# Kernel tuning notes

Measured on AMD Instinct MI355X. Metric: run time of the kernel, lower is better.

Reference implementation:

```python
import jax, jax.numpy as jnp
import numpy as np

N_ATOMS = 200000
N_EDGES = 6400000
N_TYPES = 4
COULOMB = 14.399645478425668  # e^2 / (4 pi eps0) in eV*Angstrom
P_EXP = 0.23
A0 = 0.4685


def _phi(r, c, da):
    # r: (E,), c: (4,), da: (4, E) -> (E,)
    return jnp.sum(c[:, None] * jnp.exp(-r * da), axis=0)


def _dphi(r, c, da):
    return jnp.sum(-c[:, None] * da * jnp.exp(-r * da), axis=0)


def _d2phi(r, c, da):
    return jnp.sum(c[:, None] * da ** 2 * jnp.exp(-r * da), axis=0)


def setup_inputs() -> dict:
    key = jax.random.key(0)
    k1, k2, k3, k4 = jax.random.split(key, 4)
    rij = jax.random.uniform(k1, (N_EDGES,), dtype=jnp.float32) * 2.0 + 0.1
    first_atom = jax.random.randint(k2, (N_EDGES,), 0, N_ATOMS, dtype=jnp.int32)
    second_atom = jax.random.randint(k3, (N_EDGES,), 0, N_ATOMS, dtype=jnp.int32)
    atom_type_index = jax.random.randint(k4, (N_ATOMS,), 0, N_TYPES, dtype=jnp.int32)
    # ASE covalent radii for H, C, N, O (Angstrom) and atomic numbers
    covalent_radii = jnp.array([0.31, 0.76, 0.71, 0.66], dtype=jnp.float32)
    atomic_numbers = jnp.array([1.0, 6.0, 7.0, 8.0], dtype=jnp.float32)
    return {
        "rij": rij,
        "covalent_radii": covalent_radii,
        "atomic_numbers": atomic_numbers,
        "first_atom": first_atom,
        "second_atom": second_atom,
        "atom_type_index": atom_type_index,
        "n_atoms": N_ATOMS,
    }


def reference(rij, covalent_radii, atomic_numbers, first_atom, second_atom, atom_type_index, n_atoms):
    # ZBL 4-term exponential screening coefficients
    c = jnp.array([0.02817, 0.28022, 0.50986, 0.18175], dtype=rij.dtype)
    d = jnp.array([0.20162, 0.4029, 0.94229, 3.1998], dtype=rij.dtype)

    ti = atom_type_index[first_atom]   # (E,)
    tj = atom_type_index[second_atom]  # (E,)
    zi = atomic_numbers[ti]
    zj = atomic_numbers[tj]
    rc = covalent_radii[ti] + covalent_radii[tj]  # outer cutoff per pair

    a = A0 / (zi ** P_EXP + zj ** P_EXP)  # (E,)
    da = d[:, None] / a                    # (4, E)
    factor = COULOMB * zi * zj             # (E,)

    # energy at rij
    e = factor / rij * _phi(rij, c, da)

    # switching polynomial matched at rc (r1 = 0)
    phi_c = _phi(rc, c, da)
    dphi_c = _dphi(rc, c, da)
    d2phi_c = _d2phi(rc, c, da)
    ec = factor / rc * phi_c
    dec = factor / rc * (-phi_c / rc + dphi_c)
    d2ec = factor / rc * (d2phi_c - 2.0 / rc * dphi_c + 2.0 * phi_c / rc ** 2)

    A = (-3.0 * dec + rc * d2ec) / rc ** 2
    B = (2.0 * dec - rc * d2ec) / rc ** 3
    C = -ec + rc * dec / 2.0 - rc * rc * d2ec / 12.0

    e = e + A / 3.0 * rij ** 3 + B / 4.0 * rij ** 4 + C
    e = e / 2.0
    e = jnp.where(rij > rc, jnp.zeros_like(e), e)

    # scatter pair energies onto first atom of each pair
    e_nodes = jax.ops.segment_sum(e, first_atom, num_segments=n_atoms)
    return e_nodes
```

## Files before the change

### kernel.cpp

```cpp
#include <hip/hip_runtime.h>

#define TPB_PACK  256
#define P1_BLOCKS 512
#define P1_TPB    512
#define BUCKET_BITS 10
#define BS (1 << BUCKET_BITS)
#define P2_TPB    256
#define P2_S      8
#define CMAX      64
#define NB_MAX    256

__global__ __launch_bounds__(TPB_PACK) void zbl_pack(
    const int* __restrict__ types, unsigned int* __restrict__ packed,
    int natoms, int nwords)
{
    int w = blockIdx.x * TPB_PACK + threadIdx.x;
    if (w >= nwords) return;
    int base = w << 4;
    unsigned int word = 0;
    #pragma unroll
    for (int j = 0; j < 16; ++j) {
        int i = base + j;
        unsigned int t = (i < natoms) ? (unsigned int)types[i] : 0u;
        word |= (t & 3u) << (2 * j);
    }
    packed[w] = word;
}

__global__ __launch_bounds__(P1_TPB) void zbl_bin(
    const float* __restrict__ rij,
    const float* __restrict__ rcov,
    const float* __restrict__ znum,
    const int*  __restrict__ fa,
    const int*  __restrict__ sa,
    const unsigned int* __restrict__ packed,
    int2*  __restrict__ regions,
    int*   __restrict__ counts,
    float* __restrict__ fallback,
    int E, int nquad, int natoms, int nwords, int NB, int C, int chunkQ)
{
    extern __shared__ unsigned int s_packed[];
    __shared__ float tab[9][16];
    __shared__ int scnt[NB_MAX];

    for (int w = threadIdx.x; w < nwords; w += P1_TPB)
        s_packed[w] = packed[w];
    for (int t = threadIdx.x; t < NB; t += P1_TPB) scnt[t] = 0;

    if (threadIdx.x < 16) {
        const float cc[4] = {0.02817f, 0.28022f, 0.50986f, 0.18175f};
        const float dd[4] = {0.20162f, 0.4029f, 0.94229f, 3.1998f};
        const float COUL = 14.399645478425668f;
        int t = threadIdx.x;
        int ti = t >> 2, tj = t & 3;
        float zi = znum[ti], zj = znum[tj];
        float rc = rcov[ti] + rcov[tj];
        float a = 0.4685f / (powf(zi, 0.23f) + powf(zj, 0.23f));
        float inva = 1.0f / a;
        float factor = COUL * zi * zj;
        float da[4], ee[4];
        float phi = 0.0f, dphi = 0.0f, d2phi = 0.0f;
        #pragma unroll
        for (int k = 0; k < 4; ++k) {
            da[k] = dd[k] * inva;
            ee[k] = expf(-rc * da[k]);
            phi   += cc[k] * ee[k];
            dphi  -= cc[k] * da[k] * ee[k];
            d2phi += cc[k] * da[k] * da[k] * ee[k];
        }
        float invrc = 1.0f / rc;
        float ec   = factor * invrc * phi;
        float dec  = factor * invrc * (-phi * invrc + dphi);
        float d2ec = factor * invrc * (d2phi - 2.0f * invrc * dphi + 2.0f * phi * invrc * invrc);
        float A = (-3.0f * dec + rc * d2ec) * invrc * invrc;
        float B = (2.0f * dec - rc * d2ec) * invrc * invrc * invrc;
        float Cc = -ec + 0.5f * rc * dec - rc * rc * d2ec * (1.0f / 12.0f);
        const float L2E = 1.4426950408889634f;
        tab[0][t] = 0.5f * factor;
        tab[1][t] = rc;
        tab[2][t] = -da[0] * L2E;
        tab[3][t] = -da[1] * L2E;
        tab[4][t] = -da[2] * L2E;
        tab[5][t] = -da[3] * L2E;
        tab[6][t] = A * (1.0f / 6.0f);
        tab[7][t] = B * 0.125f;
        tab[8][t] = Cc * 0.5f;
    }
    __syncthreads();

    const float lc0 = -5.1497481f;
    const float lc1 = -1.8353434f;
    const float lc2 = -0.9718340f;
    const float lc3 = -2.4600449f;

    const float4* rij4 = (const float4*)rij;
    const int4*   fa4  = (const int4*)fa;
    const int4*   sa4  = (const int4*)sa;

    int q0 = blockIdx.x * chunkQ;
    int q1 = q0 + chunkQ; if (q1 > nquad) q1 = nquad;

    for (int q = q0 + threadIdx.x; q < q1; q += P1_TPB) {
        float4 rv = rij4[q];
        int4   iv = fa4[q];
        int4   jv = sa4[q];
        float ra[4] = {rv.x, rv.y, rv.z, rv.w};
        int   ia[4] = {iv.x, iv.y, iv.z, iv.w};
        int   ja[4] = {jv.x, jv.y, jv.z, jv.w};
        int   ta[4];
        #pragma unroll
        for (int k = 0; k < 4; ++k) {
            int i = ia[k], j = ja[k];
            unsigned int wi = s_packed[i >> 4], wj = s_packed[j >> 4];
            unsigned int ti = (wi >> ((i & 15) * 2)) & 3u;
            unsigned int tj = (wj >> ((j & 15) * 2)) & 3u;
            ta[k] = (int)((ti << 2) | tj);
        }
        #pragma unroll
        for (int k = 0; k < 4; ++k) {
            int t = ta[k];
            float r = ra[k];
            if (r <= tab[1][t]) {
                float p = __builtin_amdgcn_exp2f(__builtin_fmaf(r, tab[2][t], lc0))
                        + __builtin_amdgcn_exp2f(__builtin_fmaf(r, tab[3][t], lc1))
                        + __builtin_amdgcn_exp2f(__builtin_fmaf(r, tab[4][t], lc2))
                        + __builtin_amdgcn_exp2f(__builtin_fmaf(r, tab[5][t], lc3));
                float r3 = r * r * r;
                float poly = __builtin_fmaf(__builtin_fmaf(tab[7][t], r, tab[6][t]), r3, tab[8][t]);
                float e = __builtin_fmaf(tab[0][t] * p, __builtin_amdgcn_rcpf(r), poly);
                int atom = ia[k];
                int b = atom >> BUCKET_BITS;
                int slot = atomicAdd(&scnt[b], 1);
                if (slot < C)
                    regions[((size_t)blockIdx.x * NB + b) * (size_t)C + slot] =
                        make_int2(__float_as_int(e), atom);
                else
                    unsafeAtomicAdd(&fallback[atom], e);
            }
        }
    }

    if (blockIdx.x == 0) {
        for (int idx = nquad * 4 + threadIdx.x; idx < E; idx += P1_TPB) {
            int i = fa[idx], j = sa[idx];
            unsigned int wi = s_packed[i >> 4], wj = s_packed[j >> 4];
            int t = (int)((((wi >> ((i & 15) * 2)) & 3u) << 2) |
                           ((wj >> ((j & 15) * 2)) & 3u));
            float r = rij[idx];
            if (r <= tab[1][t]) {
                float p = __builtin_amdgcn_exp2f(__builtin_fmaf(r, tab[2][t], lc0))
                        + __builtin_amdgcn_exp2f(__builtin_fmaf(r, tab[3][t], lc1))
                        + __builtin_amdgcn_exp2f(__builtin_fmaf(r, tab[4][t], lc2))
                        + __builtin_amdgcn_exp2f(__builtin_fmaf(r, tab[5][t], lc3));
                float r3 = r * r * r;
                float poly = __builtin_fmaf(__builtin_fmaf(tab[7][t], r, tab[6][t]), r3, tab[8][t]);
                float e = __builtin_fmaf(tab[0][t] * p, __builtin_amdgcn_rcpf(r), poly);
                int b = i >> BUCKET_BITS;
                int slot = atomicAdd(&scnt[b], 1);
                if (slot < C)
                    regions[((size_t)blockIdx.x * NB + b) * (size_t)C + slot] =
                        make_int2(__float_as_int(e), i);
                else
                    unsafeAtomicAdd(&fallback[i], e);
            }
        }
    }

    __syncthreads();
    if (C > 0)
        for (int t = threadIdx.x; t < NB; t += P1_TPB)
            counts[t * P1_BLOCKS + blockIdx.x] = min(scnt[t], C);
}

__global__ __launch_bounds__(P2_TPB) void zbl_agg(
    const int2* __restrict__ regions,
    const int*  __restrict__ counts,
    const float* __restrict__ fallback,
    float* __restrict__ out,
    int natoms, int NB, int C)
{
    const int PPS = P1_BLOCKS / P2_S;
    __shared__ float acc[BS];
    __shared__ int s_n[PPS];

    int b = blockIdx.x;
    int s = blockIdx.y;
    if (threadIdx.x < PPS)
        s_n[threadIdx.x] = counts[b * P1_BLOCKS + s + P2_S * threadIdx.x];
    for (int i = threadIdx.x; i < BS; i += P2_TPB) acc[i] = 0.0f;
    __syncthreads();

    int wave = threadIdx.x >> 6;
    int lane = threadIdx.x & 63;
    for (int pi = wave; pi < PPS; pi += (P2_TPB >> 6)) {
        int n = s_n[pi];
        int p = s + P2_S * pi;
        if (lane < n) {
            int2 r = regions[((size_t)p * NB + b) * (size_t)C + lane];
            atomicAdd(&acc[r.y & (BS - 1)], __int_as_float(r.x));
        }
    }
    __syncthreads();

    int abase = b << BUCKET_BITS;
    for (int i = threadIdx.x; i < BS; i += P2_TPB) {
        int atom = abase + i;
        if (atom < natoms) {
            float v = acc[i];
            if (s == 0) v += fallback[atom];
            unsafeAtomicAdd(&out[atom], v);
        }
    }
}

extern "C" void kernel_launch(void* const* d_in, const int* in_sizes, int n_in,
                              void* d_out, int out_size, void* d_ws, size_t ws_size,
                              hipStream_t stream) {
    const float* rij  = (const float*)d_in[0];
    const float* rcov = (const float*)d_in[1];
    const float* znum = (const float*)d_in[2];
    const int*   fa   = (const int*)d_in[3];
    const int*   sa   = (const int*)d_in[4];
    const int*   types= (const int*)d_in[5];
    float* out = (float*)d_out;
    int E = in_sizes[0];
    int natoms = out_size;
    int nquad = E / 4;
    int nwords = (natoms + 15) / 16;
    int NB = (natoms + BS - 1) >> BUCKET_BITS;
    if (NB > NB_MAX) NB = NB_MAX;
    int chunkQ = (nquad + P1_BLOCKS - 1) / P1_BLOCKS;

    size_t packed_bytes = ((size_t)nwords * 4 + 255) & ~(size_t)255;
    size_t cnt_bytes    = ((size_t)NB * P1_BLOCKS * 4 + 255) & ~(size_t)255;
    size_t fb_bytes     = ((size_t)natoms * 4 + 255) & ~(size_t)255;
    unsigned int* packed = (unsigned int*)d_ws;
    int*   counts   = (int*)((char*)d_ws + packed_bytes);
    float* fallback = (float*)((char*)d_ws + packed_bytes + cnt_bytes);
    int2*  regions  = (int2*)((char*)d_ws + packed_bytes + cnt_bytes + fb_bytes);

    long long avail = (long long)ws_size - (long long)(packed_bytes + cnt_bytes + fb_bytes);
    int C = 0;
    if (avail > 0) C = (int)(avail / ((long long)P1_BLOCKS * (long long)NB * 8));
    if (C > CMAX) C = CMAX;

    size_t smem = (size_t)nwords * sizeof(unsigned int);

    zbl_pack<<<(nwords + TPB_PACK - 1) / TPB_PACK, TPB_PACK, 0, stream>>>(
        types, packed, natoms, nwords);

    if (C >= 1) {
        hipMemsetAsync(fallback, 0, fb_bytes, stream);
        hipMemsetAsync(d_out, 0, (size_t)natoms * 4, stream);
        zbl_bin<<<P1_BLOCKS, P1_TPB, smem, stream>>>(
            rij, rcov, znum, fa, sa, packed, regions, counts, fallback,
            E, nquad, natoms, nwords, NB, C, chunkQ);
        dim3 g2(NB, P2_S);
        zbl_agg<<<g2, P2_TPB, 0, stream>>>(
            regions, counts, fallback, out, natoms, NB, C);
    } else {
        hipMemsetAsync(d_out, 0, (size_t)natoms * 4, stream);
        zbl_bin<<<P1_BLOCKS, P1_TPB, smem, stream>>>(
            rij, rcov, znum, fa, sa, packed, regions, counts, out,
            E, nquad, natoms, nwords, NB, 0, chunkQ);
    }
}
```

Before: 188.8 us.

## Pack bin records into 32-bit words, split producers, add deterministic reduction pass

Each binned record now packs the energy with its low 10 mantissa bits rounded off and replaced by the atom's in-bucket index, halving region traffic. The binning kernel runs more blocks, and each block keeps two per-wave-group counter sets, so there are more producer regions and less LDS atomic contention. Aggregation writes per-slice partials instead of doing global atomic adds, and a new reduction kernel sums the partials plus the fallback, which removes the output memset. In exchange, energy precision is lost in the low mantissa bits and an extra kernel launch is added.

```diff
diff --git a/kernel.cpp b/kernel.cpp
--- a/kernel.cpp
+++ b/kernel.cpp
@@ -1,13 +1,17 @@
 #include <hip/hip_runtime.h>
 
 #define TPB_PACK  256
-#define P1_BLOCKS 512
+#define P1_BLOCKS 768
 #define P1_TPB    512
+#define REP       2
+#define PRODUCERS (P1_BLOCKS * REP)
 #define BUCKET_BITS 10
 #define BS (1 << BUCKET_BITS)
 #define P2_TPB    256
 #define P2_S      8
-#define CMAX      64
+#define PPS       (PRODUCERS / P2_S)
+#define TPB_RED   256
+#define CMAX      48
 #define NB_MAX    256
 
 __global__ __launch_bounds__(TPB_PACK) void zbl_pack(
@@ -34,18 +38,18 @@
     const int*  __restrict__ fa,
     const int*  __restrict__ sa,
     const unsigned int* __restrict__ packed,
-    int2*  __restrict__ regions,
+    unsigned int* __restrict__ regions,
     int*   __restrict__ counts,
     float* __restrict__ fallback,
     int E, int nquad, int natoms, int nwords, int NB, int C, int chunkQ)
 {
     extern __shared__ unsigned int s_packed[];
     __shared__ float tab[9][16];
-    __shared__ int scnt[NB_MAX];
+    __shared__ int scnt[REP * NB_MAX];
 
     for (int w = threadIdx.x; w < nwords; w += P1_TPB)
         s_packed[w] = packed[w];
-    for (int t = threadIdx.x; t < NB; t += P1_TPB) scnt[t] = 0;
+    for (int t = threadIdx.x; t < REP * NB; t += P1_TPB) scnt[t] = 0;
 
     if (threadIdx.x < 16) {
         const float cc[4] = {0.02817f, 0.28022f, 0.50986f, 0.18175f};
@@ -97,6 +101,9 @@
     const int4*   fa4  = (const int4*)fa;
     const int4*   sa4  = (const int4*)sa;
 
+    int rep = (threadIdx.x >> 6) & (REP - 1);
+    int vp  = blockIdx.x * REP + rep;
+
     int q0 = blockIdx.x * chunkQ;
     int q1 = q0 + chunkQ; if (q1 > nquad) q1 = nquad;
 
@@ -130,12 +137,14 @@
                 float e = __builtin_fmaf(tab[0][t] * p, __builtin_amdgcn_rcpf(r), poly);
                 int atom = ia[k];
                 int b = atom >> BUCKET_BITS;
-                int slot = atomicAdd(&scnt[b], 1);
-                if (slot < C)
-                    regions[((size_t)blockIdx.x * NB + b) * (size_t)C + slot] =
-                        make_int2(__float_as_int(e), atom);
-                else
+                int slot = atomicAdd(&scnt[rep * NB + b], 1);
+                if (slot < C) {
+                    unsigned rec = ((__float_as_uint(e) + 0x200u) & 0xFFFFFC00u)
+                                 | (unsigned)(atom & (BS - 1));
+                    regions[((size_t)vp * NB + b) * (size_t)C + slot] = rec;
+                } else {
                     unsafeAtomicAdd(&fallback[atom], e);
+                }
             }
         }
     }
@@ -156,61 +165,76 @@
                 float poly = __builtin_fmaf(__builtin_fmaf(tab[7][t], r, tab[6][t]), r3, tab[8][t]);
                 float e = __builtin_fmaf(tab[0][t] * p, __builtin_amdgcn_rcpf(r), poly);
                 int b = i >> BUCKET_BITS;
-                int slot = atomicAdd(&scnt[b], 1);
-                if (slot < C)
-                    regions[((size_t)blockIdx.x * NB + b) * (size_t)C + slot] =
-                        make_int2(__float_as_int(e), i);
-                else
+                int slot = atomicAdd(&scnt[rep * NB + b], 1);
+                if (slot < C) {
+                    unsigned rec = ((__float_as_uint(e) + 0x200u) & 0xFFFFFC00u)
+                                 | (unsigned)(i & (BS - 1));
+                    regions[((size_t)vp * NB + b) * (size_t)C + slot] = rec;
+                } else {
                     unsafeAtomicAdd(&fallback[i], e);
+                }
             }
         }
     }
 
     __syncthreads();
-    if (C > 0)
-        for (int t = threadIdx.x; t < NB; t += P1_TPB)
-            counts[t * P1_BLOCKS + blockIdx.x] = min(scnt[t], C);
+    if (C > 0) {
+        for (int t = threadIdx.x; t < REP * NB; t += P1_TPB) {
+            int rr = t / NB, b = t - rr * NB;
+            counts[(size_t)b * PRODUCERS + blockIdx.x * REP + rr] = min(scnt[t], C);
+        }
+    }
 }
 
 __global__ __launch_bounds__(P2_TPB) void zbl_agg(
-    const int2* __restrict__ regions,
+    const unsigned int* __restrict__ regions,
     const int*  __restrict__ counts,
-    const float* __restrict__ fallback,
-    float* __restrict__ out,
-    int natoms, int NB, int C)
-{
-    const int PPS = P1_BLOCKS / P2_S;
+    float* __restrict__ partials,
+    int NB, int C)
+{
     __shared__ float acc[BS];
     __shared__ int s_n[PPS];
 
     int b = blockIdx.x;
     int s = blockIdx.y;
-    if (threadIdx.x < PPS)
-        s_n[threadIdx.x] = counts[b * P1_BLOCKS + s + P2_S * threadIdx.x];
     for (int i = threadIdx.x; i < BS; i += P2_TPB) acc[i] = 0.0f;
+    for (int pi = threadIdx.x; pi < PPS; pi += P2_TPB)
+        s_n[pi] = counts[(size_t)b * PRODUCERS + pi * P2_S + s];
     __syncthreads();
 
     int wave = threadIdx.x >> 6;
     int lane = threadIdx.x & 63;
     for (int pi = wave; pi < PPS; pi += (P2_TPB >> 6)) {
         int n = s_n[pi];
-        int p = s + P2_S * pi;
-        if (lane < n) {
-            int2 r = regions[((size_t)p * NB + b) * (size_t)C + lane];
-            atomicAdd(&acc[r.y & (BS - 1)], __int_as_float(r.x));
-        }
-    }
-    __syncthreads();
-
-    int abase = b << BUCKET_BITS;
-    for (int i = threadIdx.x; i < BS; i += P2_TPB) {
-        int atom = abase + i;
-        if (atom < natoms) {
-            float v = acc[i];
-            if (s == 0) v += fallback[atom];
-            unsafeAtomicAdd(&out[atom], v);
-        }
-    }
+        int vp = pi * P2_S + s;
+        size_t base = ((size_t)vp * NB + b) * (size_t)C;
+        for (int t = lane; t < n; t += 64) {
+            unsigned rec = regions[base + t];
+            atomicAdd(&acc[rec & (BS - 1)],
+                      __uint_as_float(rec & ~(unsigned)(BS - 1)));
+        }
+    }
+    __syncthreads();
+
+    float* dst = partials + ((size_t)b * P2_S + s) * BS;
+    for (int i = threadIdx.x; i < BS; i += P2_TPB)
+        dst[i] = acc[i];
+}
+
+__global__ __launch_bounds__(TPB_RED) void zbl_red(
+    const float* __restrict__ partials,
+    const float* __restrict__ fallback,
+    float* __restrict__ out,
+    int natoms)
+{
+    int atom = blockIdx.x * TPB_RED + threadIdx.x;
+    if (atom >= natoms) return;
+    int b = atom >> BUCKET_BITS, i = atom & (BS - 1);
+    float s = fallback[atom];
+    const float* p = partials + (size_t)b * P2_S * BS + i;
+    #pragma unroll
+    for (int k = 0; k < P2_S; ++k) s += p[(size_t)k * BS];
+    out[atom] = s;
 }
 
 extern "C" void kernel_launch(void* const* d_in, const int* in_sizes, int n_in,
@@ -228,20 +252,23 @@
     int nquad = E / 4;
     int nwords = (natoms + 15) / 16;
     int NB = (natoms + BS - 1) >> BUCKET_BITS;
-    if (NB > NB_MAX) NB = NB_MAX;
     int chunkQ = (nquad + P1_BLOCKS - 1) / P1_BLOCKS;
 
     size_t packed_bytes = ((size_t)nwords * 4 + 255) & ~(size_t)255;
-    size_t cnt_bytes    = ((size_t)NB * P1_BLOCKS * 4 + 255) & ~(size_t)255;
+    size_t cnt_bytes    = ((size_t)NB * PRODUCERS * 4 + 255) & ~(size_t)255;
     size_t fb_bytes     = ((size_t)natoms * 4 + 255) & ~(size_t)255;
+    size_t part_bytes   = ((size_t)NB * P2_S * BS * 4 + 255) & ~(size_t)255;
     unsigned int* packed = (unsigned int*)d_ws;
-    int*   counts   = (int*)((char*)d_ws + packed_bytes);
+    int*   counts   = (int*)  ((char*)d_ws + packed_bytes);
     float* fallback = (float*)((char*)d_ws + packed_bytes + cnt_bytes);
-    int2*  regions  = (int2*)((char*)d_ws + packed_bytes + cnt_bytes + fb_bytes);
-
-    long long avail = (long long)ws_size - (long long)(packed_bytes + cnt_bytes + fb_bytes);
+    float* partials = (float*)((char*)d_ws + packed_bytes + cnt_bytes + fb_bytes);
+    unsigned int* regions = (unsigned int*)((char*)d_ws + packed_bytes + cnt_bytes
+                                            + fb_bytes + part_bytes);
+
+    long long avail = (long long)ws_size
+                    - (long long)(packed_bytes + cnt_bytes + fb_bytes + part_bytes);
     int C = 0;
-    if (avail > 0) C = (int)(avail / ((long long)P1_BLOCKS * (long long)NB * 8));
+    if (avail > 0) C = (int)(avail / ((long long)PRODUCERS * (long long)NB * 4));
     if (C > CMAX) C = CMAX;
 
     size_t smem = (size_t)nwords * sizeof(unsigned int);
@@ -249,15 +276,15 @@
     zbl_pack<<<(nwords + TPB_PACK - 1) / TPB_PACK, TPB_PACK, 0, stream>>>(
         types, packed, natoms, nwords);
 
-    if (C >= 1) {
+    if (C >= 4) {
         hipMemsetAsync(fallback, 0, fb_bytes, stream);
-        hipMemsetAsync(d_out, 0, (size_t)natoms * 4, stream);
         zbl_bin<<<P1_BLOCKS, P1_TPB, smem, stream>>>(
             rij, rcov, znum, fa, sa, packed, regions, counts, fallback,
             E, nquad, natoms, nwords, NB, C, chunkQ);
         dim3 g2(NB, P2_S);
-        zbl_agg<<<g2, P2_TPB, 0, stream>>>(
-            regions, counts, fallback, out, natoms, NB, C);
+        zbl_agg<<<g2, P2_TPB, 0, stream>>>(regions, counts, partials, NB, C);
+        zbl_red<<<(natoms + TPB_RED - 1) / TPB_RED, TPB_RED, 0, stream>>>(
+            partials, fallback, out, natoms);
     } else {
         hipMemsetAsync(d_out, 0, (size_t)natoms * 4, stream);
         zbl_bin<<<P1_BLOCKS, P1_TPB, smem, stream>>>(
```

Result: slower. 220.4 us (+16.7%).

## Bin edges into coarse 16K-atom superbuckets with wave-aggregated slot reservation

Applied to the files above, without the earlier changes.

Edges now go into 13 superbuckets of 16K atoms instead of 196 buckets of 1024 atoms, and each block gets a capacity of up to 896 records per superbucket. Slot reservation uses a per-wave ballot and prefix count, so each wave issues one LDS atomic per superbucket instead of one per lane. Aggregation builds 64KB shared-memory histograms per (superbucket, subset) and writes partials, which a separate reduction kernel sums with the fallback into the output. This removes the output memset and global atomics on the output, but adds a 13-iteration ballot loop per edge, a larger LDS footprint, and an extra kernel launch.

```diff
diff --git a/kernel.cpp b/kernel.cpp
--- a/kernel.cpp
+++ b/kernel.cpp
@@ -3,12 +3,13 @@
 #define TPB_PACK  256
 #define P1_BLOCKS 512
 #define P1_TPB    512
-#define BUCKET_BITS 10
-#define BS (1 << BUCKET_BITS)
-#define P2_TPB    256
-#define P2_S      8
-#define CMAX      64
-#define NB_MAX    256
+#define SB_BITS   14
+#define SBS       (1 << SB_BITS)
+#define NS_MAX    16
+#define P2_TPB    1024
+#define R_SUB     40
+#define TPB_RED   256
+#define CAP_MAX   896
 
 __global__ __launch_bounds__(TPB_PACK) void zbl_pack(
     const int* __restrict__ types, unsigned int* __restrict__ packed,
@@ -37,15 +38,15 @@
     int2*  __restrict__ regions,
     int*   __restrict__ counts,
     float* __restrict__ fallback,
-    int E, int nquad, int natoms, int nwords, int NB, int C, int chunkQ)
+    int E, int nquad, int natoms, int nwords, int NS, int cap, int chunkQ)
 {
     extern __shared__ unsigned int s_packed[];
     __shared__ float tab[9][16];
-    __shared__ int scnt[NB_MAX];
+    __shared__ int scnt[NS_MAX];
 
     for (int w = threadIdx.x; w < nwords; w += P1_TPB)
         s_packed[w] = packed[w];
-    for (int t = threadIdx.x; t < NB; t += P1_TPB) scnt[t] = 0;
+    if (threadIdx.x < NS) scnt[threadIdx.x] = 0;
 
     if (threadIdx.x < 16) {
         const float cc[4] = {0.02817f, 0.28022f, 0.50986f, 0.18175f};
@@ -97,6 +98,8 @@
     const int4*   fa4  = (const int4*)fa;
     const int4*   sa4  = (const int4*)sa;
 
+    size_t myreg = (size_t)blockIdx.x * NS;
+
     int q0 = blockIdx.x * chunkQ;
     int q1 = q0 + chunkQ; if (q1 > nquad) q1 = nquad;
 
@@ -120,22 +123,38 @@
         for (int k = 0; k < 4; ++k) {
             int t = ta[k];
             float r = ra[k];
-            if (r <= tab[1][t]) {
+            int atom = ia[k];
+            bool pass = (r <= tab[1][t]);
+            float e = 0.0f;
+            if (pass) {
                 float p = __builtin_amdgcn_exp2f(__builtin_fmaf(r, tab[2][t], lc0))
                         + __builtin_amdgcn_exp2f(__builtin_fmaf(r, tab[3][t], lc1))
                         + __builtin_amdgcn_exp2f(__builtin_fmaf(r, tab[4][t], lc2))
                         + __builtin_amdgcn_exp2f(__builtin_fmaf(r, tab[5][t], lc3));
                 float r3 = r * r * r;
                 float poly = __builtin_fmaf(__builtin_fmaf(tab[7][t], r, tab[6][t]), r3, tab[8][t]);
-                float e = __builtin_fmaf(tab[0][t] * p, __builtin_amdgcn_rcpf(r), poly);
-                int atom = ia[k];
-                int b = atom >> BUCKET_BITS;
-                int slot = atomicAdd(&scnt[b], 1);
-                if (slot < C)
-                    regions[((size_t)blockIdx.x * NB + b) * (size_t)C + slot] =
-                        make_int2(__float_as_int(e), atom);
-                else
-                    unsafeAtomicAdd(&fallback[atom], e);
+                e = __builtin_fmaf(tab[0][t] * p, __builtin_amdgcn_rcpf(r), poly);
+            }
+            int sb = atom >> SB_BITS;
+            for (int s = 0; s < NS; ++s) {
+                bool mine = pass && (sb == s);
+                unsigned long long m = __ballot(mine);
+                if (m == 0ull) continue;
+                int prefix = __builtin_amdgcn_mbcnt_hi((unsigned)(m >> 32),
+                             __builtin_amdgcn_mbcnt_lo((unsigned)m, 0));
+                int leader = __ffsll((unsigned long long)m) - 1;
+                int base0 = 0;
+                if (mine && prefix == 0)
+                    base0 = atomicAdd(&scnt[s], __popcll(m));
+                int base = __shfl(base0, leader);
+                if (mine) {
+                    int slot = base + prefix;
+                    if (slot < cap)
+                        regions[(myreg + s) * (size_t)cap + slot] =
+                            make_int2(__float_as_int(e), atom);
+                    else
+                        unsafeAtomicAdd(&fallback[atom], e);
+                }
             }
         }
     }
@@ -155,62 +174,56 @@
                 float r3 = r * r * r;
                 float poly = __builtin_fmaf(__builtin_fmaf(tab[7][t], r, tab[6][t]), r3, tab[8][t]);
                 float e = __builtin_fmaf(tab[0][t] * p, __builtin_amdgcn_rcpf(r), poly);
-                int b = i >> BUCKET_BITS;
-                int slot = atomicAdd(&scnt[b], 1);
-                if (slot < C)
-                    regions[((size_t)blockIdx.x * NB + b) * (size_t)C + slot] =
-                        make_int2(__float_as_int(e), i);
-                else
-                    unsafeAtomicAdd(&fallback[i], e);
+                unsafeAtomicAdd(&fallback[i], e);
             }
         }
     }
 
     __syncthreads();
-    if (C > 0)
-        for (int t = threadIdx.x; t < NB; t += P1_TPB)
-            counts[t * P1_BLOCKS + blockIdx.x] = min(scnt[t], C);
+    if (cap > 0 && threadIdx.x < NS)
+        counts[threadIdx.x * P1_BLOCKS + blockIdx.x] = min(scnt[threadIdx.x], cap);
 }
 
 __global__ __launch_bounds__(P2_TPB) void zbl_agg(
     const int2* __restrict__ regions,
     const int*  __restrict__ counts,
+    float* __restrict__ partials,
+    int NS, int cap)
+{
+    __shared__ float acc[SBS];
+    int s = blockIdx.x;
+    int r = blockIdx.y;
+    for (int i = threadIdx.x; i < SBS; i += P2_TPB) acc[i] = 0.0f;
+    __syncthreads();
+
+    for (int p = r; p < P1_BLOCKS; p += R_SUB) {
+        int n = counts[s * P1_BLOCKS + p];
+        size_t base = ((size_t)p * NS + s) * (size_t)cap;
+        for (int t = threadIdx.x; t < n; t += P2_TPB) {
+            int2 rec = regions[base + t];
+            atomicAdd(&acc[rec.y & (SBS - 1)], __int_as_float(rec.x));
+        }
+    }
+    __syncthreads();
+
+    float* dst = partials + ((size_t)s * R_SUB + r) * SBS;
+    for (int i = threadIdx.x; i < SBS; i += P2_TPB)
+        dst[i] = acc[i];
+}
+
+__global__ __launch_bounds__(TPB_RED) void zbl_red(
+    const float* __restrict__ partials,
     const float* __restrict__ fallback,
     float* __restrict__ out,
-    int natoms, int NB, int C)
-{
-    const int PPS = P1_BLOCKS / P2_S;
-    __shared__ float acc[BS];
-    __shared__ int s_n[PPS];
-
-    int b = blockIdx.x;
-    int s = blockIdx.y;
-    if (threadIdx.x < PPS)
-        s_n[threadIdx.x] = counts[b * P1_BLOCKS + s + P2_S * threadIdx.x];
-    for (int i = threadIdx.x; i < BS; i += P2_TPB) acc[i] = 0.0f;
-    __syncthreads();
-
-    int wave = threadIdx.x >> 6;
-    int lane = threadIdx.x & 63;
-    for (int pi = wave; pi < PPS; pi += (P2_TPB >> 6)) {
-        int n = s_n[pi];
-        int p = s + P2_S * pi;
-        if (lane < n) {
-            int2 r = regions[((size_t)p * NB + b) * (size_t)C + lane];
-            atomicAdd(&acc[r.y & (BS - 1)], __int_as_float(r.x));
-        }
-    }
-    __syncthreads();
-
-    int abase = b << BUCKET_BITS;
-    for (int i = threadIdx.x; i < BS; i += P2_TPB) {
-        int atom = abase + i;
-        if (atom < natoms) {
-            float v = acc[i];
-            if (s == 0) v += fallback[atom];
-            unsafeAtomicAdd(&out[atom], v);
-        }
-    }
+    int natoms)
+{
+    int atom = blockIdx.x * TPB_RED + threadIdx.x;
+    if (atom >= natoms) return;
+    int s = atom >> SB_BITS, i = atom & (SBS - 1);
+    float acc = fallback[atom];
+    const float* p = partials + (size_t)s * R_SUB * SBS + i;
+    for (int k = 0; k < R_SUB; ++k) acc += p[(size_t)k * SBS];
+    out[atom] = acc;
 }
 
 extern "C" void kernel_launch(void* const* d_in, const int* in_sizes, int n_in,
@@ -227,41 +240,45 @@
     int natoms = out_size;
     int nquad = E / 4;
     int nwords = (natoms + 15) / 16;
-    int NB = (natoms + BS - 1) >> BUCKET_BITS;
-    if (NB > NB_MAX) NB = NB_MAX;
+    int NS = (natoms + SBS - 1) >> SB_BITS;
+    if (NS > NS_MAX) NS = NS_MAX;
     int chunkQ = (nquad + P1_BLOCKS - 1) / P1_BLOCKS;
 
     size_t packed_bytes = ((size_t)nwords * 4 + 255) & ~(size_t)255;
-    size_t cnt_bytes    = ((size_t)NB * P1_BLOCKS * 4 + 255) & ~(size_t)255;
+    size_t cnt_bytes    = ((size_t)NS * P1_BLOCKS * 4 + 255) & ~(size_t)255;
     size_t fb_bytes     = ((size_t)natoms * 4 + 255) & ~(size_t)255;
+    size_t part_bytes   = ((size_t)NS * R_SUB * SBS * 4 + 255) & ~(size_t)255;
     unsigned int* packed = (unsigned int*)d_ws;
-    int*   counts   = (int*)((char*)d_ws + packed_bytes);
+    int*   counts   = (int*)  ((char*)d_ws + packed_bytes);
     float* fallback = (float*)((char*)d_ws + packed_bytes + cnt_bytes);
-    int2*  regions  = (int2*)((char*)d_ws + packed_bytes + cnt_bytes + fb_bytes);
-
-    long long avail = (long long)ws_size - (long long)(packed_bytes + cnt_bytes + fb_bytes);
-    int C = 0;
-    if (avail > 0) C = (int)(avail / ((long long)P1_BLOCKS * (long long)NB * 8));
-    if (C > CMAX) C = CMAX;
+    float* partials = (float*)((char*)d_ws + packed_bytes + cnt_bytes + fb_bytes);
+    int2*  regions  = (int2*) ((char*)d_ws + packed_bytes + cnt_bytes
+                               + fb_bytes + part_bytes);
+
+    long long avail = (long long)ws_size
+                    - (long long)(packed_bytes + cnt_bytes + fb_bytes + part_bytes);
+    int cap = 0;
+    if (avail > 0) cap = (int)(avail / ((long long)P1_BLOCKS * (long long)NS * 8));
+    if (cap > CAP_MAX) cap = CAP_MAX;
 
     size_t smem = (size_t)nwords * sizeof(unsigned int);
 
     zbl_pack<<<(nwords + TPB_PACK - 1) / TPB_PACK, TPB_PACK, 0, stream>>>(
         types, packed, natoms, nwords);
 
-    if (C >= 1) {
+    if (cap >= 64) {
         hipMemsetAsync(fallback, 0, fb_bytes, stream);
-        hipMemsetAsync(d_out, 0, (size_t)natoms * 4, stream);
         zbl_bin<<<P1_BLOCKS, P1_TPB, smem, stream>>>(
             rij, rcov, znum, fa, sa, packed, regions, counts, fallback,
-            E, nquad, natoms, nwords, NB, C, chunkQ);
-        dim3 g2(NB, P2_S);
-        zbl_agg<<<g2, P2_TPB, 0, stream>>>(
-            regions, counts, fallback, out, natoms, NB, C);
+            E, nquad, natoms, nwords, NS, cap, chunkQ);
+        dim3 g2(NS, R_SUB);
+        zbl_agg<<<g2, P2_TPB, 0, stream>>>(regions, counts, partials, NS, cap);
+        zbl_red<<<(natoms + TPB_RED - 1) / TPB_RED, TPB_RED, 0, stream>>>(
+            partials, fallback, out, natoms);
     } else {
         hipMemsetAsync(d_out, 0, (size_t)natoms * 4, stream);
         zbl_bin<<<P1_BLOCKS, P1_TPB, smem, stream>>>(
             rij, rcov, znum, fa, sa, packed, regions, counts, out,
-            E, nquad, natoms, nwords, NB, 0, chunkQ);
-    }
-}
+            E, nquad, natoms, nwords, NS, 0, chunkQ);
+    }
+}
```

New measurement: 209.6 us. +11.0%, slower.
